# Kernel optimization log

Measured on AMD Instinct MI355X. Metric: run time of the kernel, lower is better.

The kernel has to match this reference:

```python
import jax, jax.numpy as jnp
import numpy as np

STRIDES = (8, 16, 32)
H = W = 640
SCORE_T = 0.5
NMS_T = 0.4


def setup_inputs() -> dict:
    key = jax.random.key(0)
    ks = jax.random.split(key, 9)
    feats = [(H // s) * (W // s) for s in STRIDES]  # 6400, 1600, 400
    d = {}
    for i, n in enumerate(feats):
        d[f"score{i}"] = jax.random.normal(ks[i], (1, n, 1), jnp.float32)
        d[f"bbox{i}"] = jax.random.normal(ks[3 + i], (1, n, 4), jnp.float32)
        d[f"kps{i}"] = jax.random.normal(ks[6 + i], (1, n, 10), jnp.float32)
    return d


def _anchors(stride):
    fh, fw = H // stride, W // stride
    yv, xv = jnp.meshgrid(jnp.arange(fh), jnp.arange(fw), indexing="ij")
    return jnp.stack([xv, yv], -1).reshape(-1, 2).astype(jnp.float32) * stride


def _decode(score, bbox, kps, stride):
    pts = _anchors(stride)                      # [N,2]
    s = jax.nn.sigmoid(score[0]).reshape(-1)    # [N]
    d = bbox[0] * stride                        # [N,4]
    x1 = pts[:, 0] - d[:, 0]
    y1 = pts[:, 1] - d[:, 1]
    x2 = pts[:, 0] + d[:, 2]
    y2 = pts[:, 1] + d[:, 3]
    b = jnp.stack([x1, y1, x2, y2], -1)         # [N,4]
    kd = (kps[0] * stride).reshape(-1, 5, 2)    # [N,5,2] (px,py pairs)
    k = (pts[:, None, :] + kd).reshape(-1, 10)  # [N,10]
    return s, b, k


def _iou(b):
    area = (b[:, 2] - b[:, 0]) * (b[:, 3] - b[:, 1])
    lt = jnp.maximum(b[:, None, :2], b[None, :, :2])
    rb = jnp.minimum(b[:, None, 2:], b[None, :, 2:])
    wh = jnp.clip(rb - lt, 0.0)
    inter = wh[..., 0] * wh[..., 1]
    return inter / (area[:, None] + area[None, :] - inter + 1e-9)


def _nms_keep(iou, valid, thresh):
    # greedy NMS on score-sorted boxes: keep i iff no earlier kept j has IoU>thresh
    n = valid.shape[0]
    def body(keep, xs):
        i, row = xs
        suppressed = jnp.any(keep & (row > thresh))
        keep = keep.at[i].set(valid[i] & ~suppressed)
        return keep, None
    keep, _ = jax.lax.scan(body, jnp.zeros(n, bool), (jnp.arange(n), iou))
    return keep


def reference(score0, score1, score2, bbox0, bbox1, bbox2, kps0, kps1, kps2):
    parts = [
        _decode(s, b, k, st)
        for s, b, k, st in zip(
            (score0, score1, score2), (bbox0, bbox1, bbox2), (kps0, kps1, kps2), STRIDES
        )
    ]
    scores = jnp.concatenate([p[0] for p in parts])  # [8400]
    boxes = jnp.concatenate([p[1] for p in parts])   # [8400,4]
    kpss = jnp.concatenate([p[2] for p in parts])    # [8400,10]
    order = jnp.argsort(-scores)                     # score-descending (NMS order)
    scores = scores[order]
    boxes = boxes[order]
    kpss = kpss[order]
    valid = scores > SCORE_T                         # threshold mask
    iou = _iou(jax.lax.stop_gradient(boxes))         # [8400,8400] ~282MB
    keep = _nms_keep(iou, valid, NMS_T)
    m = keep.astype(boxes.dtype)
    # fixed-shape equivalent of dynamic gather: suppressed rows zeroed, keep mask returned
    return boxes * m[:, None], scores * m, kpss * m[:, None], keep
```

## Files before the change

kernel.cpp:

```cpp
#include <hip/hip_runtime.h>
#include <math.h>

#define N_TOT 8400
#define MASK_WORDS 132
#define CAP 32
#define RT 33
#define NBP 256

typedef unsigned long long u64;

__device__ __forceinline__ unsigned mono_u32(float f) {
    unsigned u = __float_as_uint(f);
    return (u & 0x80000000u) ? ~u : (u | 0x80000000u);
}

#define WS_SLOGIT  0
#define WS_SBOX    33600
#define WS_CNT     168000
#define WS_ROWFLAG 201600
#define WS_DIAG    202672
#define WS_ENT     270256
#define WS_PARTIAL 4571056

__global__ __launch_bounds__(256) void rank_partial_kernel(
        const float* __restrict__ score0, const float* __restrict__ score1,
        const float* __restrict__ score2, int* __restrict__ partial) {
    __shared__ u64 tile[256];
    const int tid = threadIdx.x;
    const int bi = blockIdx.x, bj = blockIdx.y;

    int j = bj * 256 + tid;
    u64 kj = ~0ull;
    if (j < N_TOT) {
        const float* sc; int m;
        if (j < 6400)      { sc = score0; m = j; }
        else if (j < 8000) { sc = score1; m = j - 6400; }
        else               { sc = score2; m = j - 8000; }
        kj = ((u64)(~mono_u32(sc[m])) << 14) | (u64)j;
    }
    tile[tid] = kj;
    __syncthreads();

    int i = bi * 256 + tid;
    if (i >= N_TOT) return;
    const float* sc; int m;
    if (i < 6400)      { sc = score0; m = i; }
    else if (i < 8000) { sc = score1; m = i - 6400; }
    else               { sc = score2; m = i - 8000; }
    u64 ki = ((u64)(~mono_u32(sc[m])) << 14) | (u64)i;
    int rk = 0;
    #pragma unroll 8
    for (int k = 0; k < 256; ++k) rk += (tile[k] < ki) ? 1 : 0;
    partial[bj * 8448 + i] = rk;
}

__global__ __launch_bounds__(256) void decode_scatter_kernel(
        const float* __restrict__ score0, const float* __restrict__ bbox0, const float* __restrict__ kps0,
        const float* __restrict__ score1, const float* __restrict__ bbox1, const float* __restrict__ kps1,
        const float* __restrict__ score2, const float* __restrict__ bbox2, const float* __restrict__ kps2,
        const int* __restrict__ partial,
        float* __restrict__ s_logit, float* __restrict__ s_box,
        unsigned* __restrict__ cnt, u64* __restrict__ rowflag,
        float* __restrict__ out) {
    int i = blockIdx.x * 256 + threadIdx.x;
    if (i < N_TOT) cnt[i] = 0u;
    if (i < MASK_WORDS) rowflag[i] = 0ull;
    if (i >= N_TOT) return;

    int r = 0;
    #pragma unroll
    for (int b = 0; b < RT; ++b) r += partial[b * 8448 + i];

    const float *sc, *bb, *kp; int m, F; float s;
    if (i < 6400)      { sc=score0; bb=bbox0; kp=kps0; m=i;       F=80; s=8.f;  }
    else if (i < 8000) { sc=score1; bb=bbox1; kp=kps1; m=i-6400;  F=40; s=16.f; }
    else               { sc=score2; bb=bbox2; kp=kps2; m=i-8000;  F=20; s=32.f; }
    float px = (float)(m % F) * s;
    float py = (float)(m / F) * s;
    float lg = sc[m];
    float mv = (lg > 0.f) ? 1.f : 0.f;
    s_logit[r] = lg;
    float d0=bb[m*4+0]*s, d1=bb[m*4+1]*s, d2=bb[m*4+2]*s, d3=bb[m*4+3]*s;
    float x1 = px - d0, y1 = py - d1, x2 = px + d2, y2 = py + d3;
    ((float4*)s_box)[r] = make_float4(x1, y1, x2, y2);

    float* ob  = out;
    float* os  = out + 33600;
    float* okp = out + 42000;
    float* om  = out + 126000;
    ob[r*4+0]=x1*mv; ob[r*4+1]=y1*mv; ob[r*4+2]=x2*mv; ob[r*4+3]=y2*mv;
    os[r] = (1.0f / (1.0f + expf(-lg))) * mv;
    #pragma unroll
    for (int c = 0; c < 5; ++c) {
        okp[r*10 + 2*c]   = (px + kp[m*10 + 2*c]   * s) * mv;
        okp[r*10 + 2*c+1] = (py + kp[m*10 + 2*c+1] * s) * mv;
    }
    om[r] = mv;
}

__global__ __launch_bounds__(256) void pairs_kernel(
        const float* __restrict__ s_logit, const float* __restrict__ s_box,
        unsigned* __restrict__ cnt, ulonglong2* __restrict__ ent,
        u64* __restrict__ diag, u64* __restrict__ rowflag) {
    __shared__ float4 cboxS[4][64];
    __shared__ float  careaS[4][64];
    const int tid = threadIdx.x;
    const int wv = tid >> 6, lane = tid & 63;
    const int gw = blockIdx.x * 4 + wv;

    for (int t = gw; t < 132 * 67; t += NBP * 4) {
        int x = t % 132, y = t / 132;
        int rb, cw;
        if (x + y < MASK_WORDS) { rb = x; cw = x + y; }
        else if (y == MASK_WORDS / 2) continue;
        else { rb = x + y - MASK_WORDS; cw = x; }
        bool isdiag = (rb == cw);

        int j = cw * 64 + lane;
        float4 cb = make_float4(0.f, 0.f, 0.f, 0.f);
        float lgj = -1.f;
        if (j < N_TOT) {
            cb = ((const float4*)s_box)[j];
            lgj = s_logit[j];
        }
        cboxS[wv][lane] = cb;
        careaS[wv][lane] = (cb.z - cb.x) * (cb.w - cb.y);
        u64 cvalid = __ballot(j < N_TOT && lgj > 0.f);
        if (!isdiag && cvalid == 0ull) continue;

        int r = rb * 64 + lane;
        float lgr = isdiag ? lgj : ((r < N_TOT) ? s_logit[r] : -1.f);
        if (!isdiag && __ballot(lgr > 0.f) == 0ull) continue;

        u64 bits = 0ull;
        if (cvalid != 0ull && lgr > 0.f) {
            float4 rb4 = isdiag ? cb : ((const float4*)s_box)[r];
            float rarea = (rb4.z - rb4.x) * (rb4.w - rb4.y);
            #pragma unroll 4
            for (int k = 0; k < 64; ++k) {
                float4 c4 = cboxS[wv][k];
                float ltx = fmaxf(rb4.x, c4.x);
                float lty = fmaxf(rb4.y, c4.y);
                float rbx = fminf(rb4.z, c4.z);
                float rby = fminf(rb4.w, c4.w);
                float w = fmaxf(rbx - ltx, 0.f);
                float h = fmaxf(rby - lty, 0.f);
                float inter = w * h;
                float iou = inter / (rarea + careaS[wv][k] - inter + 1e-9f);
                bits |= (iou > 0.4f) ? (1ull << k) : 0ull;
            }
            u64 m = cvalid;
            if (isdiag) m &= (lane == 63) ? 0ull : (~0ull << (lane + 1));
            bits &= m;
        }
        if (isdiag) {
            if (r < N_TOT) diag[r] = bits;
            if (bits) atomicOr(&rowflag[r >> 6], 1ull << (r & 63));
            continue;
        }
        if (bits) {
            unsigned idx = atomicAdd(&cnt[r], 1u);
            if (idx < CAP) {
                ulonglong2 e; e.x = bits; e.y = (u64)cw;
                ent[(size_t)r * CAP + idx] = e;
            }
            atomicOr(&rowflag[r >> 6], 1ull << (r & 63));
        }
    }
}

__global__ __launch_bounds__(256) void nms_kernel(
        const u64* __restrict__ rowflag_g,
        const unsigned* __restrict__ cnt_g,
        const u64* __restrict__ diag_g,
        const ulonglong2* __restrict__ ent_g,
        float* __restrict__ out) {
    __shared__ u64 rem_lds[MASK_WORDS];
    __shared__ unsigned short wlist[MASK_WORDS];
    const int tid = threadIdx.x;

    for (int q = tid; q < MASK_WORDS; q += 256) rem_lds[q] = 0ull;
    __syncthreads();

    if (tid < 64) {
        int lane = tid;
        u64 rf[3];
        #pragma unroll
        for (int s = 0; s < 3; ++s) {
            int w = s * 64 + lane;
            rf[s] = (w < MASK_WORDS) ? rowflag_g[w] : 0ull;
        }
        int base = 0;
        #pragma unroll
        for (int s = 0; s < 3; ++s) {
            bool nz = rf[s] != 0ull;
            u64 bal = __ballot(nz);
            int pos = __popcll(bal & ((1ull << lane) - 1ull));
            if (nz) wlist[base + pos] = (unsigned short)(s * 64 + lane);
            base += (int)__popcll(bal);
        }
        int n_w = base;

        int wdA=0, wdB=0, wdC=0;
        unsigned cA=0u, cB=0u, cC=0u;
        u64 lbA=0ull, lbB=0ull, lbC=0ull;
        ulonglong2 A0,A1,A2,A3, B0,B1,B2,B3, C0,C1,C2,C3;
        A0.x=A0.y=0ull; A1=A0; A2=A0; A3=A0;
        B0=A0; B1=A0; B2=A0; B3=A0; C0=A0; C1=A0; C2=A0; C3=A0;

#define LOADST(t, wd, c, lb, e0, e1, e2, e3) do {              \
        wd = 0; c = 0u; lb = 0ull;                             \
        if ((t) < n_w) {                                       \
            wd = (int)wlist[t];                                \
            int row_ = wd * 64 + lane;                         \
            if (row_ < N_TOT) {                                \
                const ulonglong2* ep_ = ent_g + (size_t)row_ * CAP; \
                c  = cnt_g[row_];                              \
                lb = diag_g[row_];                             \
                e0 = ep_[0];                                   \
                e1 = ep_[1];                                   \
                e2 = ep_[2];                                   \
                e3 = ep_[3];                                   \
            }                                                  \
        }                                                      \
    } while (0)

#define STEP(wd, c, lb, e0, e1, e2, e3, TNEXT) do {            \
        u64 remw = rem_lds[wd];                                \
        u64 cand = __ballot(c > 0u || lb != 0ull) & ~remw;     \
        if (cand) {                                            \
            u64 kept;                                          \
            u64 S = __ballot(lb != 0ull) & cand;               \
            if (S == 0ull) {                                   \
                kept = cand;                                   \
            } else {                                           \
                u64 rn = remw;                                 \
                u64 pend = S;                                  \
                while (pend) {                                 \
                    int b_ = __builtin_ctzll(pend);            \
                    pend &= pend - 1ull;                       \
                    if (!((rn >> b_) & 1ull)) {                \
                        unsigned lo_ = (unsigned)__builtin_amdgcn_readlane((int)(unsigned)lb, b_); \
                        unsigned hi_ = (unsigned)__builtin_amdgcn_readlane((int)(unsigned)(lb >> 32), b_); \
                        rn |= ((u64)hi_ << 32) | (u64)lo_;     \
                        pend &= ~rn;                           \
                    }                                          \
                }                                              \
                kept = cand & ~rn;                             \
                if (lane == 0) rem_lds[wd] = rn;               \
            }                                                  \
            bool kp_ = (kept >> lane) & 1ull;                  \
            if (kp_) {                                         \
                if (c > 0u) atomicOr(&rem_lds[(int)e0.y], e0.x); \
                if (c > 1u) atomicOr(&rem_lds[(int)e1.y], e1.x); \
                if (c > 2u) atomicOr(&rem_lds[(int)e2.y], e2.x); \
                if (c > 3u) atomicOr(&rem_lds[(int)e3.y], e3.x); \
            }                                                  \
            if (__ballot(kp_ && c > 4u)) {                     \
                if (kp_ && c > 4u) {                           \
                    unsigned cm_ = min(c, (unsigned)CAP);      \
                    int row_ = wd * 64 + lane;                 \
                    for (unsigned e_ = 4; e_ < cm_; ++e_) {    \
                        ulonglong2 g_ = ent_g[(size_t)row_ * CAP + e_]; \
                        atomicOr(&rem_lds[(int)g_.y], g_.x);   \
                    }                                          \
                }                                              \
            }                                                  \
        }                                                      \
        LOADST(TNEXT, wd, c, lb, e0, e1, e2, e3);              \
    } while (0)

        if (n_w > 0) {
            LOADST(0, wdA, cA, lbA, A0, A1, A2, A3);
            LOADST(1, wdB, cB, lbB, B0, B1, B2, B3);
            LOADST(2, wdC, cC, lbC, C0, C1, C2, C3);
            int t = 0;
            while (true) {
                STEP(wdA, cA, lbA, A0, A1, A2, A3, t + 3); if (++t >= n_w) break;
                STEP(wdB, cB, lbB, B0, B1, B2, B3, t + 3); if (++t >= n_w) break;
                STEP(wdC, cC, lbC, C0, C1, C2, C3, t + 3); if (++t >= n_w) break;
            }
        }
#undef STEP
#undef LOADST
    }
    __syncthreads();

    float* ob  = out;
    float* os  = out + 33600;
    float* okp = out + 42000;
    float* om  = out + 126000;
    for (int r = tid; r < N_TOT; r += 256) {
        if ((rem_lds[r >> 6] >> (r & 63)) & 1ull) {
            om[r] = 0.f;
            os[r] = 0.f;
            ((float4*)ob)[r] = make_float4(0.f, 0.f, 0.f, 0.f);
            #pragma unroll
            for (int c = 0; c < 10; ++c) okp[r*10 + c] = 0.f;
        }
    }
}

extern "C" void kernel_launch(void* const* d_in, const int* in_sizes, int n_in,
                              void* d_out, int out_size, void* d_ws, size_t ws_size,
                              hipStream_t stream) {
    const float *score0, *bbox0, *kps0, *score1, *bbox1, *kps1, *score2, *bbox2, *kps2;
    if (in_sizes[1] == 25600) {
        score0 = (const float*)d_in[0]; bbox0 = (const float*)d_in[1]; kps0 = (const float*)d_in[2];
        score1 = (const float*)d_in[3]; bbox1 = (const float*)d_in[4]; kps1 = (const float*)d_in[5];
        score2 = (const float*)d_in[6]; bbox2 = (const float*)d_in[7]; kps2 = (const float*)d_in[8];
    } else {
        score0 = (const float*)d_in[0]; score1 = (const float*)d_in[1]; score2 = (const float*)d_in[2];
        bbox0  = (const float*)d_in[3]; bbox1  = (const float*)d_in[4]; bbox2  = (const float*)d_in[5];
        kps0   = (const float*)d_in[6]; kps1   = (const float*)d_in[7]; kps2   = (const float*)d_in[8];
    }

    char* ws = (char*)d_ws;
    float* s_logit   = (float*)(ws + WS_SLOGIT);
    float* s_box     = (float*)(ws + WS_SBOX);
    unsigned* cnt    = (unsigned*)(ws + WS_CNT);
    u64* rowflag     = (u64*)(ws + WS_ROWFLAG);
    u64* diag        = (u64*)(ws + WS_DIAG);
    ulonglong2* ent  = (ulonglong2*)(ws + WS_ENT);
    int* partial     = (int*)(ws + WS_PARTIAL);
    float* out = (float*)d_out;

    rank_partial_kernel<<<dim3(RT, RT), 256, 0, stream>>>(score0, score1, score2, partial);
    decode_scatter_kernel<<<RT, 256, 0, stream>>>(
        score0, bbox0, kps0, score1, bbox1, kps1, score2, bbox2, kps2,
        partial, s_logit, s_box, cnt, rowflag, out);
    pairs_kernel<<<NBP, 256, 0, stream>>>(s_logit, s_box, cnt, ent, diag, rowflag);
    nms_kernel<<<1, 256, 0, stream>>>(rowflag, cnt, diag, ent, out);
}
```

Baseline: 114.9 us.

## Compact NMS entry layout and precompute per-word masks to shorten serial NMS loop

Splits the per-row suppression entry list into a dense 4-entry array plus an overflow array, so the serial NMS wave reads contiguous 64-byte rows. It also precomputes per-word diagonal-source masks in the pairs kernel and caches rowflag words in LDS, so candidate and source masks are scalar reads instead of ballots. The prefetch pipeline goes from 3 to 4 stages. This adds an extra ballot and store in the pairs kernel and uses more registers in the single-block NMS kernel.

```diff
diff --git a/kernel.cpp b/kernel.cpp
--- a/kernel.cpp
+++ b/kernel.cpp
@@ -14,13 +14,26 @@
     return (u & 0x80000000u) ? ~u : (u | 0x80000000u);
 }
 
+__device__ __forceinline__ u64 rfl64(u64 v) {
+    unsigned lo = __builtin_amdgcn_readfirstlane((unsigned)v);
+    unsigned hi = __builtin_amdgcn_readfirstlane((unsigned)(v >> 32));
+    return ((u64)hi << 32) | (u64)lo;
+}
+__device__ __forceinline__ u64 rdl64(u64 v, int l) {
+    unsigned lo = (unsigned)__builtin_amdgcn_readlane((int)(unsigned)v, l);
+    unsigned hi = (unsigned)__builtin_amdgcn_readlane((int)(unsigned)(v >> 32), l);
+    return ((u64)hi << 32) | (u64)lo;
+}
+
 #define WS_SLOGIT  0
 #define WS_SBOX    33600
 #define WS_CNT     168000
 #define WS_ROWFLAG 201600
-#define WS_DIAG    202672
-#define WS_ENT     270256
-#define WS_PARTIAL 4571056
+#define WS_DSRC    202672
+#define WS_DIAG    203728
+#define WS_ENT4    271312
+#define WS_ENTOV   811984
+#define WS_PARTIAL 5112784
 
 __global__ __launch_bounds__(256) void rank_partial_kernel(
         const float* __restrict__ score0, const float* __restrict__ score1,
@@ -100,8 +113,9 @@
 
 __global__ __launch_bounds__(256) void pairs_kernel(
         const float* __restrict__ s_logit, const float* __restrict__ s_box,
-        unsigned* __restrict__ cnt, ulonglong2* __restrict__ ent,
-        u64* __restrict__ diag, u64* __restrict__ rowflag) {
+        unsigned* __restrict__ cnt, ulonglong2* __restrict__ ent4,
+        ulonglong2* __restrict__ entOv, u64* __restrict__ diag,
+        u64* __restrict__ dsrc, u64* __restrict__ rowflag) {
     __shared__ float4 cboxS[4][64];
     __shared__ float  careaS[4][64];
     const int tid = threadIdx.x;
@@ -154,131 +168,134 @@
             bits &= m;
         }
         if (isdiag) {
+            u64 dmask = __ballot(bits != 0ull);
             if (r < N_TOT) diag[r] = bits;
+            if (lane == 0) dsrc[cw] = dmask;
             if (bits) atomicOr(&rowflag[r >> 6], 1ull << (r & 63));
             continue;
         }
         if (bits) {
             unsigned idx = atomicAdd(&cnt[r], 1u);
-            if (idx < CAP) {
-                ulonglong2 e; e.x = bits; e.y = (u64)cw;
-                ent[(size_t)r * CAP + idx] = e;
-            }
+            ulonglong2 e; e.x = bits; e.y = (u64)cw;
+            if (idx < 4u)        ent4[(size_t)r * 4 + idx] = e;
+            else if (idx < CAP)  entOv[(size_t)r * CAP + idx] = e;
             atomicOr(&rowflag[r >> 6], 1ull << (r & 63));
         }
     }
 }
 
-__global__ __launch_bounds__(256) void nms_kernel(
+__global__ __launch_bounds__(256, 1) void nms_kernel(
         const u64* __restrict__ rowflag_g,
         const unsigned* __restrict__ cnt_g,
         const u64* __restrict__ diag_g,
-        const ulonglong2* __restrict__ ent_g,
+        const u64* __restrict__ dsrc_g,
+        const ulonglong2* __restrict__ ent4_g,
+        const ulonglong2* __restrict__ entOv_g,
         float* __restrict__ out) {
     __shared__ u64 rem_lds[MASK_WORDS];
+    __shared__ u64 wflag_lds[MASK_WORDS];
+    __shared__ u64 dsrc_lds[MASK_WORDS];
     __shared__ unsigned short wlist[MASK_WORDS];
     const int tid = threadIdx.x;
 
-    for (int q = tid; q < MASK_WORDS; q += 256) rem_lds[q] = 0ull;
+    for (int q = tid; q < MASK_WORDS; q += 256) {
+        rem_lds[q] = 0ull;
+        dsrc_lds[q] = dsrc_g[q];
+    }
     __syncthreads();
 
     if (tid < 64) {
-        int lane = tid;
-        u64 rf[3];
+        const int lane = tid;
+        int base = 0;
         #pragma unroll
         for (int s = 0; s < 3; ++s) {
             int w = s * 64 + lane;
-            rf[s] = (w < MASK_WORDS) ? rowflag_g[w] : 0ull;
-        }
-        int base = 0;
-        #pragma unroll
-        for (int s = 0; s < 3; ++s) {
-            bool nz = rf[s] != 0ull;
+            u64 rfv = (w < MASK_WORDS) ? rowflag_g[w] : 0ull;
+            bool nz = rfv != 0ull;
             u64 bal = __ballot(nz);
             int pos = __popcll(bal & ((1ull << lane) - 1ull));
-            if (nz) wlist[base + pos] = (unsigned short)(s * 64 + lane);
+            if (nz) { wlist[base + pos] = (unsigned short)w; wflag_lds[base + pos] = rfv; }
             base += (int)__popcll(bal);
         }
         int n_w = base;
 
-        int wdA=0, wdB=0, wdC=0;
-        unsigned cA=0u, cB=0u, cC=0u;
-        u64 lbA=0ull, lbB=0ull, lbC=0ull;
-        ulonglong2 A0,A1,A2,A3, B0,B1,B2,B3, C0,C1,C2,C3;
+        int wdA=0, wdB=0, wdC=0, wdD=0;
+        unsigned cA=0u, cB=0u, cC=0u, cD=0u;
+        u64 lbA=0ull, lbB=0ull, lbC=0ull, lbD=0ull;
+        ulonglong2 A0,A1,A2,A3, B0,B1,B2,B3, C0,C1,C2,C3, D0,D1,D2,D3;
         A0.x=A0.y=0ull; A1=A0; A2=A0; A3=A0;
         B0=A0; B1=A0; B2=A0; B3=A0; C0=A0; C1=A0; C2=A0; C3=A0;
-
-#define LOADST(t, wd, c, lb, e0, e1, e2, e3) do {              \
+        D0=A0; D1=A0; D2=A0; D3=A0;
+
+#define LOADST(t, wd, c, lb, E0, E1, E2, E3) do {              \
         wd = 0; c = 0u; lb = 0ull;                             \
         if ((t) < n_w) {                                       \
             wd = (int)wlist[t];                                \
             int row_ = wd * 64 + lane;                         \
             if (row_ < N_TOT) {                                \
-                const ulonglong2* ep_ = ent_g + (size_t)row_ * CAP; \
+                const ulonglong2* p_ = ent4_g + (size_t)row_ * 4; \
                 c  = cnt_g[row_];                              \
                 lb = diag_g[row_];                             \
-                e0 = ep_[0];                                   \
-                e1 = ep_[1];                                   \
-                e2 = ep_[2];                                   \
-                e3 = ep_[3];                                   \
+                E0 = p_[0];                                    \
+                E1 = p_[1];                                    \
+                E2 = p_[2];                                    \
+                E3 = p_[3];                                    \
             }                                                  \
         }                                                      \
     } while (0)
 
-#define STEP(wd, c, lb, e0, e1, e2, e3, TNEXT) do {            \
-        u64 remw = rem_lds[wd];                                \
-        u64 cand = __ballot(c > 0u || lb != 0ull) & ~remw;     \
-        if (cand) {                                            \
-            u64 kept;                                          \
-            u64 S = __ballot(lb != 0ull) & cand;               \
-            if (S == 0ull) {                                   \
-                kept = cand;                                   \
+#define STEP(TT, wd, c, lb, E0, E1, E2, E3, TNEXT) do {        \
+        u64 remw_ = rfl64(rem_lds[wd]);                        \
+        u64 wfl_  = rfl64(wflag_lds[TT]);                      \
+        u64 dsr_  = rfl64(dsrc_lds[wd]);                       \
+        u64 cand_ = wfl_ & ~remw_;                             \
+        if (cand_) {                                           \
+            u64 kept_;                                         \
+            u64 S_ = dsr_ & cand_;                             \
+            if (S_ == 0ull) {                                  \
+                kept_ = cand_;                                 \
             } else {                                           \
-                u64 rn = remw;                                 \
-                u64 pend = S;                                  \
-                while (pend) {                                 \
-                    int b_ = __builtin_ctzll(pend);            \
-                    pend &= pend - 1ull;                       \
-                    if (!((rn >> b_) & 1ull)) {                \
-                        unsigned lo_ = (unsigned)__builtin_amdgcn_readlane((int)(unsigned)lb, b_); \
-                        unsigned hi_ = (unsigned)__builtin_amdgcn_readlane((int)(unsigned)(lb >> 32), b_); \
-                        rn |= ((u64)hi_ << 32) | (u64)lo_;     \
-                        pend &= ~rn;                           \
+                u64 rn_ = remw_, pend_ = S_;                   \
+                while (pend_) {                                \
+                    int b_ = (int)__builtin_ctzll(pend_);      \
+                    pend_ &= pend_ - 1ull;                     \
+                    if (!((rn_ >> b_) & 1ull)) {               \
+                        rn_ |= rdl64(lb, b_);                  \
+                        pend_ &= ~rn_;                         \
                     }                                          \
                 }                                              \
-                kept = cand & ~rn;                             \
-                if (lane == 0) rem_lds[wd] = rn;               \
+                kept_ = cand_ & ~rn_;                          \
+                if (tid == 0) rem_lds[wd] = rn_;               \
             }                                                  \
-            bool kp_ = (kept >> lane) & 1ull;                  \
-            if (kp_) {                                         \
-                if (c > 0u) atomicOr(&rem_lds[(int)e0.y], e0.x); \
-                if (c > 1u) atomicOr(&rem_lds[(int)e1.y], e1.x); \
-                if (c > 2u) atomicOr(&rem_lds[(int)e2.y], e2.x); \
-                if (c > 3u) atomicOr(&rem_lds[(int)e3.y], e3.x); \
-            }                                                  \
-            if (__ballot(kp_ && c > 4u)) {                     \
-                if (kp_ && c > 4u) {                           \
+            if ((kept_ >> tid) & 1ull) {                       \
+                if (c > 0u) atomicOr(&rem_lds[(int)E0.y], E0.x); \
+                if (c > 1u) atomicOr(&rem_lds[(int)E1.y], E1.x); \
+                if (c > 2u) atomicOr(&rem_lds[(int)E2.y], E2.x); \
+                if (c > 3u) atomicOr(&rem_lds[(int)E3.y], E3.x); \
+                if (c > 4u) {                                  \
                     unsigned cm_ = min(c, (unsigned)CAP);      \
-                    int row_ = wd * 64 + lane;                 \
+                    int row_ = wd * 64 + tid;                  \
                     for (unsigned e_ = 4; e_ < cm_; ++e_) {    \
-                        ulonglong2 g_ = ent_g[(size_t)row_ * CAP + e_]; \
+                        ulonglong2 g_ = entOv_g[(size_t)row_ * CAP + e_]; \
                         atomicOr(&rem_lds[(int)g_.y], g_.x);   \
                     }                                          \
                 }                                              \
             }                                                  \
         }                                                      \
-        LOADST(TNEXT, wd, c, lb, e0, e1, e2, e3);              \
+        LOADST(TNEXT, wd, c, lb, E0, E1, E2, E3);              \
     } while (0)
 
         if (n_w > 0) {
             LOADST(0, wdA, cA, lbA, A0, A1, A2, A3);
             LOADST(1, wdB, cB, lbB, B0, B1, B2, B3);
             LOADST(2, wdC, cC, lbC, C0, C1, C2, C3);
+            LOADST(3, wdD, cD, lbD, D0, D1, D2, D3);
             int t = 0;
             while (true) {
-                STEP(wdA, cA, lbA, A0, A1, A2, A3, t + 3); if (++t >= n_w) break;
-                STEP(wdB, cB, lbB, B0, B1, B2, B3, t + 3); if (++t >= n_w) break;
-                STEP(wdC, cC, lbC, C0, C1, C2, C3, t + 3); if (++t >= n_w) break;
+                STEP(t, wdA, cA, lbA, A0, A1, A2, A3, t + 4); if (++t >= n_w) break;
+                STEP(t, wdB, cB, lbB, B0, B1, B2, B3, t + 4); if (++t >= n_w) break;
+                STEP(t, wdC, cC, lbC, C0, C1, C2, C3, t + 4); if (++t >= n_w) break;
+                STEP(t, wdD, cD, lbD, D0, D1, D2, D3, t + 4); if (++t >= n_w) break;
             }
         }
 #undef STEP
@@ -320,8 +337,10 @@
     float* s_box     = (float*)(ws + WS_SBOX);
     unsigned* cnt    = (unsigned*)(ws + WS_CNT);
     u64* rowflag     = (u64*)(ws + WS_ROWFLAG);
+    u64* dsrc        = (u64*)(ws + WS_DSRC);
     u64* diag        = (u64*)(ws + WS_DIAG);
-    ulonglong2* ent  = (ulonglong2*)(ws + WS_ENT);
+    ulonglong2* ent4 = (ulonglong2*)(ws + WS_ENT4);
+    ulonglong2* entOv= (ulonglong2*)(ws + WS_ENTOV);
     int* partial     = (int*)(ws + WS_PARTIAL);
     float* out = (float*)d_out;
 
@@ -329,6 +348,6 @@
     decode_scatter_kernel<<<RT, 256, 0, stream>>>(
         score0, bbox0, kps0, score1, bbox1, kps1, score2, bbox2, kps2,
         partial, s_logit, s_box, cnt, rowflag, out);
-    pairs_kernel<<<NBP, 256, 0, stream>>>(s_logit, s_box, cnt, ent, diag, rowflag);
-    nms_kernel<<<1, 256, 0, stream>>>(rowflag, cnt, diag, ent, out);
-}
+    pairs_kernel<<<NBP, 256, 0, stream>>>(s_logit, s_box, cnt, ent4, entOv, diag, dsrc, rowflag);
+    nms_kernel<<<1, 256, 0, stream>>>(rowflag, cnt, diag, dsrc, ent4, entOv, out);
+}
```

New measurement: 116.8 us. No clear change (+1.7%).
